# Kernel tuning notes

Measured on AMD Instinct MI355X. Metric: run time of the kernel, lower is better.

The kernel has to match this reference:

```python
import jax, jax.numpy as jnp
import numpy as np

TAU = 0.07
LAMBDA_RN = 1.0
LAMBDA_U = 1.0
BETA_FLOOR = 0.0
B = 8192


def setup_inputs() -> dict:
    key = jax.random.key(0)
    ks = jax.random.split(key, 6)
    sim_matrix = jax.random.normal(ks[0], (B, B), dtype=jnp.float32)
    alphas = jax.random.uniform(ks[1], (B,), dtype=jnp.float32)
    betas = jax.random.uniform(ks[2], (B,), dtype=jnp.float32)
    pi_a = jax.random.uniform(ks[3], (B,), dtype=jnp.float32)
    pu_weights = jax.random.uniform(ks[4], (B, B), dtype=jnp.float32)
    # PU labels in {-1, 0, +1}: RN / Unlabeled / Positive
    pu_labels = jax.random.randint(ks[5], (B,), 0, 3, dtype=jnp.int32) - 1
    return {
        "sim_matrix": sim_matrix,
        "alphas": alphas,
        "betas": betas,
        "pi_a": pi_a,
        "pu_weights": pu_weights,
        "pu_labels": pu_labels,
    }


def reference(sim_matrix, alphas, betas, pi_a, pu_weights, pu_labels):
    dt = sim_matrix.dtype
    n = sim_matrix.shape[0]
    logits = sim_matrix / TAU                      # (B, B)
    diag = jnp.eye(n, dtype=bool)
    # log Z_i over j != i
    log_Z = jax.nn.logsumexp(jnp.where(diag, -jnp.inf, logits), axis=1)  # (B,)
    centered = logits - log_Z[:, None]             # (B, B)
    ratio = jnp.exp(centered)                      # exp(logit - logZ)

    offdiag = (~diag).astype(dt)
    pos_col = (pu_labels == 1).astype(dt)[None, :]
    rn_col = (pu_labels == -1).astype(dt)[None, :]
    u_col = (pu_labels == 0).astype(dt)[None, :]

    pos_m = offdiag * pos_col                      # (B, B) float masks
    rn_m = offdiag * rn_col
    u_m = offdiag * u_col

    cnt_pos = pos_m.sum(axis=1)
    cnt_rn = rn_m.sum(axis=1)
    cnt_u = u_m.sum(axis=1)
    has_pos = cnt_pos > 0
    has_rn = cnt_rn > 0
    has_u = cnt_u > 0

    # L_pos_i = -mean_{j in P\{i}} alpha_j * (logit_ij - logZ_i)
    L_pos = -jnp.sum(pos_m * alphas[None, :] * centered, axis=1) / jnp.maximum(cnt_pos, 1.0)
    L_pos = jnp.where(has_pos, L_pos, 0.0)

    # L_rn_i = mean_{j in RN\{i}} beta_j * w_ij * exp(logit_ij - logZ_i)
    L_rn = jnp.sum(rn_m * betas[None, :] * pu_weights * ratio, axis=1) / jnp.maximum(cnt_rn, 1.0)
    L_rn = jnp.where(has_rn, L_rn, 0.0)

    # Debiased unlabeled term (nnPU)
    E_U = jnp.sum(u_m * pu_weights * ratio, axis=1) / jnp.maximum(cnt_u, 1.0)
    E_P = jnp.sum(pos_m * ratio, axis=1) / jnp.maximum(cnt_pos, 1.0)
    pi = jnp.clip(pi_a, 1e-4, 0.5)
    debiased = (E_U - pi * E_P) / (1.0 - pi + 1e-8)
    L_u = jnp.maximum(debiased, BETA_FLOOR)
    L_u = jnp.where(has_u & has_pos, L_u, 0.0)

    total_loss = jnp.mean(L_pos + LAMBDA_RN * L_rn + LAMBDA_U * L_u)
    return total_loss
```

## Files before the change

kernel.cpp:

```cpp
#include <hip/hip_runtime.h>
#include <math.h>

#define TAU 0.07f
#define INV_TAU (1.0f / TAU)
#define BLOCK 256

__global__ __launch_bounds__(BLOCK) void prep_kernel(
    const float* __restrict__ alphas, const float* __restrict__ betas,
    const int* __restrict__ labels, float* __restrict__ cvals,
    float* __restrict__ totals, int n)
{
    int j = blockIdx.x * BLOCK + threadIdx.x;
    float p = 0.f, r = 0.f, u = 0.f, sa = 0.f;
    if (j < n) {
        int lb = labels[j];
        float a = alphas[j], b = betas[j];
        float c = (lb == 1) ? a : ((lb == -1) ? b : 0.0f);
        cvals[j] = c;
        p  = (lb == 1)  ? 1.f : 0.f;
        r  = (lb == -1) ? 1.f : 0.f;
        u  = (lb == 0)  ? 1.f : 0.f;
        sa = (lb == 1)  ? a   : 0.f;
    }
    #pragma unroll
    for (int off = 1; off < 64; off <<= 1) {
        p  += __shfl_xor(p,  off);
        r  += __shfl_xor(r,  off);
        u  += __shfl_xor(u,  off);
        sa += __shfl_xor(sa, off);
    }
    if ((threadIdx.x & 63) == 0) {
        atomicAdd(&totals[0], p);
        atomicAdd(&totals[1], r);
        atomicAdd(&totals[2], u);
        atomicAdd(&totals[3], sa);
    }
}

__global__ __launch_bounds__(BLOCK) void row_kernel(
    const float* __restrict__ sim, const float* __restrict__ w,
    const float* __restrict__ cvals, const int* __restrict__ labels,
    const float* __restrict__ alphas, const float* __restrict__ pi_a,
    const float* __restrict__ totals, float* __restrict__ out, int n)
{
    const int i = blockIdx.x;
    const int t = threadIdx.x;
    const float* __restrict__ srow = sim + (size_t)i * (size_t)n;
    const float* __restrict__ wrow = w   + (size_t)i * (size_t)n;

    float m = -3.0e38f;
    float Sall = 0.f;
    float Srn  = 0.f;
    float Su   = 0.f;
    float Sp   = 0.f;
    float A    = 0.f;

    const int nv = n >> 2;
    for (int j4 = t; j4 < nv; j4 += BLOCK) {
        float4 s4 = ((const float4*)srow)[j4];
        float4 w4 = ((const float4*)wrow)[j4];
        float4 c4 = ((const float4*)cvals)[j4];
        int4   b4 = ((const int4*)labels)[j4];
        int jbase = j4 << 2;
        float ls[4]  = {s4.x * INV_TAU, s4.y * INV_TAU, s4.z * INV_TAU, s4.w * INV_TAU};
        float wv_[4] = {w4.x, w4.y, w4.z, w4.w};
        float cs[4]  = {c4.x, c4.y, c4.z, c4.w};
        int   lb_[4] = {b4.x, b4.y, b4.z, b4.w};
        #pragma unroll
        for (int q = 0; q < 4; ++q) {
            int   j     = jbase + q;
            bool  valid = (j != i);
            float l     = ls[q];
            float lv    = valid ? l : -3.0e38f;
            if (lv > m) {
                float sc = __expf(m - lv);
                Sall *= sc; Srn *= sc; Su *= sc; Sp *= sc;
                m = lv;
            }
            float e = valid ? __expf(l - m) : 0.0f;
            Sall += e;
            float te = wv_[q] * e;
            int lb = lb_[q];
            Srn += (lb == -1) ? cs[q] * te : 0.0f;
            Su  += (lb == 0)  ? te         : 0.0f;
            Sp  += (lb == 1)  ? e          : 0.0f;
            A   += (lb == 1 && valid) ? cs[q] * l : 0.0f;
        }
    }

    #pragma unroll
    for (int off = 1; off < 64; off <<= 1) {
        float m2  = __shfl_xor(m,    off);
        float Sa2 = __shfl_xor(Sall, off);
        float Sr2 = __shfl_xor(Srn,  off);
        float Su2 = __shfl_xor(Su,   off);
        float Sp2 = __shfl_xor(Sp,   off);
        float A2  = __shfl_xor(A,    off);
        float M   = fmaxf(m, m2);
        float sc1 = __expf(m  - M);
        float sc2 = __expf(m2 - M);
        Sall = Sall * sc1 + Sa2 * sc2;
        Srn  = Srn  * sc1 + Sr2 * sc2;
        Su   = Su   * sc1 + Su2 * sc2;
        Sp   = Sp   * sc1 + Sp2 * sc2;
        A   += A2;
        m    = M;
    }

    __shared__ float red[4][6];
    int wid = t >> 6, lane = t & 63;
    if (lane == 0) {
        red[wid][0] = m;  red[wid][1] = Sall; red[wid][2] = Srn;
        red[wid][3] = Su; red[wid][4] = Sp;   red[wid][5] = A;
    }
    __syncthreads();
    if (t == 0) {
        float M  = red[0][0], Sa = red[0][1], Sr = red[0][2];
        float SU = red[0][3], SP = red[0][4], AF = red[0][5];
        #pragma unroll
        for (int wv = 1; wv < 4; ++wv) {
            float m2  = red[wv][0];
            float Mn  = fmaxf(M, m2);
            float sc1 = __expf(M  - Mn);
            float sc2 = __expf(m2 - Mn);
            Sa = Sa * sc1 + red[wv][1] * sc2;
            Sr = Sr * sc1 + red[wv][2] * sc2;
            SU = SU * sc1 + red[wv][3] * sc2;
            SP = SP * sc1 + red[wv][4] * sc2;
            AF += red[wv][5];
            M   = Mn;
        }
        float logZ = M + __logf(Sa);

        int   myl  = labels[i];
        float cntP = totals[0] - ((myl == 1)  ? 1.f : 0.f);
        float cntR = totals[1] - ((myl == -1) ? 1.f : 0.f);
        float cntU = totals[2] - ((myl == 0)  ? 1.f : 0.f);
        float SAp  = totals[3] - ((myl == 1)  ? alphas[i] : 0.f);

        bool hasP = cntP > 0.f, hasR = cntR > 0.f, hasU = cntU > 0.f;
        float invSa = 1.0f / Sa;

        float Lpos = hasP ? -(AF - logZ * SAp) / fmaxf(cntP, 1.f) : 0.f;
        float Lrn  = hasR ? (Sr * invSa) / fmaxf(cntR, 1.f) : 0.f;
        float EU = (SU * invSa) / fmaxf(cntU, 1.f);
        float EP = (SP * invSa) / fmaxf(cntP, 1.f);
        float pi = fminf(fmaxf(pi_a[i], 1e-4f), 0.5f);
        float deb = (EU - pi * EP) / (1.0f - pi + 1e-8f);
        float Lu = fmaxf(deb, 0.0f);
        if (!(hasU && hasP)) Lu = 0.f;

        float loss = Lpos + Lrn + Lu;
        atomicAdd(out, loss * (1.0f / (float)n));
    }
}

extern "C" void kernel_launch(void* const* d_in, const int* in_sizes, int n_in,
                              void* d_out, int out_size, void* d_ws, size_t ws_size,
                              hipStream_t stream) {
    const float* sim    = (const float*)d_in[0];
    const float* alphas = (const float*)d_in[1];
    const float* betas  = (const float*)d_in[2];
    const float* pi_a   = (const float*)d_in[3];
    const float* w      = (const float*)d_in[4];
    const int*   labels = (const int*)d_in[5];
    float* out = (float*)d_out;
    int n = in_sizes[1];

    float* totals = (float*)d_ws;
    float* cvals  = (float*)((char*)d_ws + 256);

    hipMemsetAsync(d_ws, 0, 256, stream);
    hipMemsetAsync(d_out, 0, sizeof(float), stream);

    int nb = (n + BLOCK - 1) / BLOCK;
    prep_kernel<<<nb, BLOCK, 0, stream>>>(alphas, betas, labels, cvals, totals, n);
    row_kernel<<<n, BLOCK, 0, stream>>>(sim, w, cvals, labels, alphas, pi_a, totals, out, n);
}
```

Baseline: 541.3 us.

## Replace online-max softmax with fixed-shift exp2 and pack labels into coefficients

Drops the per-element running-max rescaling in the row reduction. It uses a constant shift of 88 with exp2, so every partial sum can be added plainly, both inside the loop and in the wave/block reductions. Labels and alpha/beta are packed into one signed code array, which removes one stream of loads per element. The diagonal term is no longer masked in the loop and is subtracted once at the end instead. The constant shift is only safe while logits stay in a bounded range; larger similarity values would overflow or underflow the exponentials.

```diff
diff --git a/kernel.cpp b/kernel.cpp
--- a/kernel.cpp
+++ b/kernel.cpp
@@ -4,10 +4,12 @@
 #define TAU 0.07f
 #define INV_TAU (1.0f / TAU)
 #define BLOCK 256
+#define SHIFT 88.0f
+#define LOG2E 1.44269504088896f
 
 __global__ __launch_bounds__(BLOCK) void prep_kernel(
     const float* __restrict__ alphas, const float* __restrict__ betas,
-    const int* __restrict__ labels, float* __restrict__ cvals,
+    const int* __restrict__ labels, float* __restrict__ code,
     float* __restrict__ totals, int n)
 {
     int j = blockIdx.x * BLOCK + threadIdx.x;
@@ -15,8 +17,8 @@
     if (j < n) {
         int lb = labels[j];
         float a = alphas[j], b = betas[j];
-        float c = (lb == 1) ? a : ((lb == -1) ? b : 0.0f);
-        cvals[j] = c;
+        float c = (lb == 1) ? (a + 2.0f) : ((lb == -1) ? -(b + 2.0f) : 0.0f);
+        code[j] = c;
         p  = (lb == 1)  ? 1.f : 0.f;
         r  = (lb == -1) ? 1.f : 0.f;
         u  = (lb == 0)  ? 1.f : 0.f;
@@ -39,8 +41,7 @@
 
 __global__ __launch_bounds__(BLOCK) void row_kernel(
     const float* __restrict__ sim, const float* __restrict__ w,
-    const float* __restrict__ cvals, const int* __restrict__ labels,
-    const float* __restrict__ alphas, const float* __restrict__ pi_a,
+    const float* __restrict__ code, const float* __restrict__ pi_a,
     const float* __restrict__ totals, float* __restrict__ out, int n)
 {
     const int i = blockIdx.x;
@@ -48,95 +49,98 @@
     const float* __restrict__ srow = sim + (size_t)i * (size_t)n;
     const float* __restrict__ wrow = w   + (size_t)i * (size_t)n;
 
-    float m = -3.0e38f;
-    float Sall = 0.f;
-    float Srn  = 0.f;
-    float Su   = 0.f;
-    float Sp   = 0.f;
-    float A    = 0.f;
+    const float k1 = INV_TAU * LOG2E;
+    const float k0 = -SHIFT * LOG2E;
+
+    float sall[4] = {0.f, 0.f, 0.f, 0.f};
+    float srn_[4] = {0.f, 0.f, 0.f, 0.f};
+    float su_[4]  = {0.f, 0.f, 0.f, 0.f};
+    float sp_[4]  = {0.f, 0.f, 0.f, 0.f};
+    float aa_[4]  = {0.f, 0.f, 0.f, 0.f};
 
     const int nv = n >> 2;
+    #pragma unroll 4
     for (int j4 = t; j4 < nv; j4 += BLOCK) {
         float4 s4 = ((const float4*)srow)[j4];
         float4 w4 = ((const float4*)wrow)[j4];
-        float4 c4 = ((const float4*)cvals)[j4];
-        int4   b4 = ((const int4*)labels)[j4];
-        int jbase = j4 << 2;
-        float ls[4]  = {s4.x * INV_TAU, s4.y * INV_TAU, s4.z * INV_TAU, s4.w * INV_TAU};
-        float wv_[4] = {w4.x, w4.y, w4.z, w4.w};
-        float cs[4]  = {c4.x, c4.y, c4.z, c4.w};
-        int   lb_[4] = {b4.x, b4.y, b4.z, b4.w};
+        float4 c4 = ((const float4*)code)[j4];
+        float ss[4] = {s4.x, s4.y, s4.z, s4.w};
+        float ws[4] = {w4.x, w4.y, w4.z, w4.w};
+        float cs[4] = {c4.x, c4.y, c4.z, c4.w};
         #pragma unroll
         for (int q = 0; q < 4; ++q) {
-            int   j     = jbase + q;
-            bool  valid = (j != i);
-            float l     = ls[q];
-            float lv    = valid ? l : -3.0e38f;
-            if (lv > m) {
-                float sc = __expf(m - lv);
-                Sall *= sc; Srn *= sc; Su *= sc; Sp *= sc;
-                m = lv;
-            }
-            float e = valid ? __expf(l - m) : 0.0f;
-            Sall += e;
-            float te = wv_[q] * e;
-            int lb = lb_[q];
-            Srn += (lb == -1) ? cs[q] * te : 0.0f;
-            Su  += (lb == 0)  ? te         : 0.0f;
-            Sp  += (lb == 1)  ? e          : 0.0f;
-            A   += (lb == 1 && valid) ? cs[q] * l : 0.0f;
+            float s  = ss[q];
+            float e  = exp2f(fmaf(s, k1, k0));
+            float l  = s * INV_TAU;
+            float te = ws[q] * e;
+            float cd = cs[q];
+            bool isRN = cd < -1.f;
+            bool isP  = cd > 1.f;
+            float c   = fabsf(cd) - 2.0f;
+            sall[q] += e;
+            srn_[q]  = fmaf(isRN ? c : 0.f, te, srn_[q]);
+            su_[q]  += (isRN || isP) ? 0.f : te;
+            sp_[q]  += isP ? e : 0.f;
+            aa_[q]   = fmaf(isP ? c : 0.f, l, aa_[q]);
         }
     }
 
+    float Sall = (sall[0] + sall[1]) + (sall[2] + sall[3]);
+    float Srn  = (srn_[0] + srn_[1]) + (srn_[2] + srn_[3]);
+    float Su   = (su_[0]  + su_[1])  + (su_[2]  + su_[3]);
+    float Sp   = (sp_[0]  + sp_[1])  + (sp_[2]  + sp_[3]);
+    float A    = (aa_[0]  + aa_[1])  + (aa_[2]  + aa_[3]);
+
     #pragma unroll
     for (int off = 1; off < 64; off <<= 1) {
-        float m2  = __shfl_xor(m,    off);
-        float Sa2 = __shfl_xor(Sall, off);
-        float Sr2 = __shfl_xor(Srn,  off);
-        float Su2 = __shfl_xor(Su,   off);
-        float Sp2 = __shfl_xor(Sp,   off);
-        float A2  = __shfl_xor(A,    off);
-        float M   = fmaxf(m, m2);
-        float sc1 = __expf(m  - M);
-        float sc2 = __expf(m2 - M);
-        Sall = Sall * sc1 + Sa2 * sc2;
-        Srn  = Srn  * sc1 + Sr2 * sc2;
-        Su   = Su   * sc1 + Su2 * sc2;
-        Sp   = Sp   * sc1 + Sp2 * sc2;
-        A   += A2;
-        m    = M;
+        Sall += __shfl_xor(Sall, off);
+        Srn  += __shfl_xor(Srn,  off);
+        Su   += __shfl_xor(Su,   off);
+        Sp   += __shfl_xor(Sp,   off);
+        A    += __shfl_xor(A,    off);
     }
 
-    __shared__ float red[4][6];
+    __shared__ float red[4][5];
     int wid = t >> 6, lane = t & 63;
     if (lane == 0) {
-        red[wid][0] = m;  red[wid][1] = Sall; red[wid][2] = Srn;
-        red[wid][3] = Su; red[wid][4] = Sp;   red[wid][5] = A;
+        red[wid][0] = Sall; red[wid][1] = Srn; red[wid][2] = Su;
+        red[wid][3] = Sp;   red[wid][4] = A;
     }
     __syncthreads();
     if (t == 0) {
-        float M  = red[0][0], Sa = red[0][1], Sr = red[0][2];
-        float SU = red[0][3], SP = red[0][4], AF = red[0][5];
+        float Sa = red[0][0], Sr = red[0][1], SU = red[0][2];
+        float SP = red[0][3], AF = red[0][4];
         #pragma unroll
         for (int wv = 1; wv < 4; ++wv) {
-            float m2  = red[wv][0];
-            float Mn  = fmaxf(M, m2);
-            float sc1 = __expf(M  - Mn);
-            float sc2 = __expf(m2 - Mn);
-            Sa = Sa * sc1 + red[wv][1] * sc2;
-            Sr = Sr * sc1 + red[wv][2] * sc2;
-            SU = SU * sc1 + red[wv][3] * sc2;
-            SP = SP * sc1 + red[wv][4] * sc2;
-            AF += red[wv][5];
-            M   = Mn;
+            Sa += red[wv][0]; Sr += red[wv][1]; SU += red[wv][2];
+            SP += red[wv][3]; AF += red[wv][4];
         }
-        float logZ = M + __logf(Sa);
 
-        int   myl  = labels[i];
+        float sii   = srow[i];
+        float wii   = wrow[i];
+        float codei = code[i];
+        float lii   = sii * INV_TAU;
+        float eii   = exp2f(fmaf(sii, k1, k0));
+        Sa -= eii;
+        int myl;
+        float alpha_i = 0.f;
+        if (codei > 1.f) {
+            myl = 1; alpha_i = codei - 2.0f;
+            SP -= eii; AF -= alpha_i * lii;
+        } else if (codei < -1.f) {
+            myl = -1;
+            Sr -= (-codei - 2.0f) * wii * eii;
+        } else {
+            myl = 0;
+            SU -= wii * eii;
+        }
+
+        float logZ = SHIFT + logf(Sa);
+
         float cntP = totals[0] - ((myl == 1)  ? 1.f : 0.f);
         float cntR = totals[1] - ((myl == -1) ? 1.f : 0.f);
         float cntU = totals[2] - ((myl == 0)  ? 1.f : 0.f);
-        float SAp  = totals[3] - ((myl == 1)  ? alphas[i] : 0.f);
+        float SAp  = totals[3] - ((myl == 1)  ? alpha_i : 0.f);
 
         bool hasP = cntP > 0.f, hasR = cntR > 0.f, hasU = cntU > 0.f;
         float invSa = 1.0f / Sa;
@@ -168,12 +172,12 @@
     int n = in_sizes[1];
 
     float* totals = (float*)d_ws;
-    float* cvals  = (float*)((char*)d_ws + 256);
+    float* code   = (float*)((char*)d_ws + 256);
 
     hipMemsetAsync(d_ws, 0, 256, stream);
     hipMemsetAsync(d_out, 0, sizeof(float), stream);
 
     int nb = (n + BLOCK - 1) / BLOCK;
-    prep_kernel<<<nb, BLOCK, 0, stream>>>(alphas, betas, labels, cvals, totals, n);
-    row_kernel<<<n, BLOCK, 0, stream>>>(sim, w, cvals, labels, alphas, pi_a, totals, out, n);
+    prep_kernel<<<nb, BLOCK, 0, stream>>>(alphas, betas, labels, code, totals, n);
+    row_kernel<<<n, BLOCK, 0, stream>>>(sim, w, code, pi_a, totals, out, n);
 }
```

Measured after the change: 558.3 us. 1.03x slower.
